# Performance work log

Measured on AMD Instinct MI355X. Metric: run time of the kernel, lower is better.

Reference implementation:

```python
import jax, jax.numpy as jnp
import numpy as np

B, T, D = 4, 4096, 768      # batch, tokens, n_embd
S = 1024                    # memory_slots (divides T -> adaptive pool == window mean)
K = 8                       # memory_topk
RW = 0.1                    # memory_retrieval_weight


def setup_inputs() -> dict:
    key = jax.random.key(0)
    ks = jax.random.split(key, 10)
    w = 1.0 / np.sqrt(D).astype(np.float32)
    return {
        "x": jax.random.normal(ks[0], (B, T, D), jnp.float32),
        "Wq": jax.random.normal(ks[1], (D, D), jnp.float32) * w,
        "bq": jnp.zeros((D,), jnp.float32),
        "Wk": jax.random.normal(ks[2], (D, D), jnp.float32) * w,
        "bk": jnp.zeros((D,), jnp.float32),
        "Wv": jax.random.normal(ks[3], (D, D), jnp.float32) * w,
        "bv": jnp.zeros((D,), jnp.float32),
        "Wp": jax.random.normal(ks[4], (D, D), jnp.float32) * w,
        "bp": jnp.zeros((D,), jnp.float32),
        "persistent_memory": jax.random.normal(ks[5], (S, D), jnp.float32),
    }


def reference(x, Wq, bq, Wk, bk, Wv, bv, Wp, bp, persistent_memory):
    # _build_memory_slots: adaptive_avg_pool1d to S slots; T % S == 0 so it is a window mean
    pooled = x.reshape(B, S, T // S, D).mean(axis=2)                    # [B,S,D]
    pers = jnp.broadcast_to(persistent_memory[None], (B, S, D))         # persistent bank
    slots = jnp.concatenate([pooled, pers], axis=1)                     # [B,2S,D]

    q = x @ Wq + bq                                                     # [B,T,D]
    k = slots @ Wk + bk                                                 # [B,2S,D]
    v = slots @ Wv + bv                                                 # [B,2S,D]

    scores = jnp.einsum('btd,bsd->bts', q, k) / jnp.sqrt(jnp.float32(D))  # [B,T,2S]
    top_s, top_i = jax.lax.top_k(scores, K)                             # [B,T,K]
    w = jax.nn.softmax(top_s, axis=-1)                                  # softmax over top-k only

    # gather top-k values: [B,T,K,D]
    vg = jnp.take_along_axis(v, top_i.reshape(B, T * K)[:, :, None], axis=1)
    vg = vg.reshape(B, T, K, D)
    retrieved = jnp.einsum('btk,btkd->btd', w, vg)                      # weighted combine

    return RW * (retrieved @ Wp + bp)                                   # proj * retrieval_weight
```

## Files before the change

kernel.cpp:

```cpp
#include <hip/hip_runtime.h>
#include <math.h>

#define BB 4
#define TT 4096
#define DD 768
#define SS 1024
#define S2 2048
#define KTOP 8
#define RWEIGHT 0.1f
#define TAU 2e-4f
#define AMB_CAP 256

typedef __attribute__((ext_vector_type(8))) _Float16 f16x8;
typedef __attribute__((ext_vector_type(4))) float f32x4;
typedef _Float16 f16;

__global__ __launch_bounds__(256) void build_pooled_all(
    const float* __restrict__ x, float* __restrict__ slots)
{
    int i = blockIdx.x * 256 + threadIdx.x;
    int s2 = i / DD;
    int d = i - s2 * DD;
    int b = s2 >> 10, s = s2 & 1023;
    const float* xb = x + (size_t)b * TT * DD + (size_t)(4 * s) * DD + d;
    slots[i] = 0.25f * (xb[0] + xb[DD] + xb[2 * DD] + xb[3 * DD]);
}

__global__ __launch_bounds__(256) void transpose_split(
    const float* __restrict__ W0, const float* __restrict__ W1,
    const float* __restrict__ W2, const float* __restrict__ W3,
    f16* __restrict__ WQh, f16* __restrict__ WQm,
    f16* __restrict__ WKh, f16* __restrict__ WKm,
    f16* __restrict__ WVh, f16* __restrict__ WPh,
    float* __restrict__ WkT32)
{
    const int z = blockIdx.z;
    const float* W = (z == 0) ? W0 : (z == 1) ? W1 : (z == 2) ? W2 : W3;
    __shared__ float t[32][33];
    int bx = blockIdx.x * 32, by = blockIdx.y * 32;
    int lx = threadIdx.x & 31, ly = threadIdx.x >> 5;
#pragma unroll
    for (int r = 0; r < 32; r += 8)
        t[ly + r][lx] = W[(size_t)(bx + ly + r) * 768 + by + lx];
    __syncthreads();
#pragma unroll
    for (int r = 0; r < 32; r += 8) {
        float w = t[lx][ly + r];
        size_t idx = (size_t)(by + ly + r) * 768 + bx + lx;
        f16 h = (f16)w;
        if (z == 0) { WQh[idx] = h; WQm[idx] = (f16)(w - (float)h); }
        else if (z == 1) { WKh[idx] = h; WKm[idx] = (f16)(w - (float)h); WkT32[idx] = w; }
        else if (z == 2) { WVh[idx] = h; }
        else { WPh[idx] = h; }
    }
}

__global__ void zeroN(int* p) { p[threadIdx.x] = 0; }

__device__ __forceinline__ void tile_split_prod(
    const float* __restrict__ A, int arow0,
    const f16* __restrict__ Bh, const f16* __restrict__ Bm, int bncol,
    const float* __restrict__ bias,
    f16* __restrict__ Ch, f16* __restrict__ Cm, int crow0,
    f16* LAh, f16* LAm, f16* LBh, f16* LBm)
{
    const int tid = threadIdx.x;
    const int lane = tid & 63;
    const int wc = (tid >> 6) & 1;
    const int wr = (tid >> 7) & 1;
    const int srow = tid >> 1, c0 = tid & 1;
    const int p0 = c0 ^ (srow & 3) ^ ((srow >> 2) & 1);
    const int wo0 = srow * 32 + p0 * 8, wo1 = wo0 ^ 16;
    const int csw = (((lane >> 4) ^ (lane & 3) ^ ((lane >> 2) & 1)) * 8);
    const size_t bn = (size_t)bncol;

    f32x4 acc[4][4];
#pragma unroll
    for (int i = 0; i < 4; ++i)
#pragma unroll
        for (int j = 0; j < 4; ++j) acc[i][j] = (f32x4){0.f, 0.f, 0.f, 0.f};

    const float* pa = A + (size_t)(arow0 + srow) * 768 + c0 * 8;
    const f16* pbh = Bh + (bn + srow) * 768 + c0 * 8;
    const f16* pbm = Bm + (bn + srow) * 768 + c0 * 8;

    for (int k0 = 0; k0 < 768; k0 += 32) {
        float4 a0 = *(const float4*)(pa + k0);
        float4 a1 = *(const float4*)(pa + k0 + 4);
        float4 a2 = *(const float4*)(pa + k0 + 16);
        float4 a3 = *(const float4*)(pa + k0 + 20);
        f16x8 bh0 = *(const f16x8*)(pbh + k0);
        f16x8 bh1 = *(const f16x8*)(pbh + k0 + 16);
        f16x8 bm0 = *(const f16x8*)(pbm + k0);
        f16x8 bm1 = *(const f16x8*)(pbm + k0 + 16);
        __syncthreads();
        {
            float av[16] = {a0.x, a0.y, a0.z, a0.w, a1.x, a1.y, a1.z, a1.w,
                            a2.x, a2.y, a2.z, a2.w, a3.x, a3.y, a3.z, a3.w};
            f16x8 h, m;
#pragma unroll
            for (int j = 0; j < 8; ++j) {
                f16 hh = (f16)av[j]; h[j] = hh; m[j] = (f16)(av[j] - (float)hh);
            }
            *(f16x8*)&LAh[wo0] = h; *(f16x8*)&LAm[wo0] = m;
#pragma unroll
            for (int j = 0; j < 8; ++j) {
                f16 hh = (f16)av[j + 8]; h[j] = hh; m[j] = (f16)(av[j + 8] - (float)hh);
            }
            *(f16x8*)&LAh[wo1] = h; *(f16x8*)&LAm[wo1] = m;
            *(f16x8*)&LBh[wo0] = bh0; *(f16x8*)&LBh[wo1] = bh1;
            *(f16x8*)&LBm[wo0] = bm0; *(f16x8*)&LBm[wo1] = bm1;
        }
        __syncthreads();

        f16x8 fah[4], fam[4], fbh[4], fbm[4];
#pragma unroll
        for (int mi = 0; mi < 4; ++mi) {
            int off = (wr * 64 + mi * 16 + (lane & 15)) * 32 + csw;
            fah[mi] = *(const f16x8*)&LAh[off];
            fam[mi] = *(const f16x8*)&LAm[off];
        }
#pragma unroll
        for (int ni = 0; ni < 4; ++ni) {
            int off = (wc * 64 + ni * 16 + (lane & 15)) * 32 + csw;
            fbh[ni] = *(const f16x8*)&LBh[off];
            fbm[ni] = *(const f16x8*)&LBm[off];
        }
#pragma unroll
        for (int mi = 0; mi < 4; ++mi)
#pragma unroll
            for (int ni = 0; ni < 4; ++ni) {
                acc[mi][ni] = __builtin_amdgcn_mfma_f32_16x16x32_f16(
                    fah[mi], fbh[ni], acc[mi][ni], 0, 0, 0);
                acc[mi][ni] = __builtin_amdgcn_mfma_f32_16x16x32_f16(
                    fah[mi], fbm[ni], acc[mi][ni], 0, 0, 0);
                acc[mi][ni] = __builtin_amdgcn_mfma_f32_16x16x32_f16(
                    fam[mi], fbh[ni], acc[mi][ni], 0, 0, 0);
            }
    }

    const int orow0 = wr * 64 + (lane >> 4) * 4;
    const int ocol0 = wc * 64 + (lane & 15);
#pragma unroll
    for (int mi = 0; mi < 4; ++mi)
#pragma unroll
        for (int ni = 0; ni < 4; ++ni) {
            size_t col = bn + ocol0 + ni * 16;
            float badd = bias[col];
            size_t rbase = (size_t)crow0 + orow0 + mi * 16;
#pragma unroll
            for (int r = 0; r < 4; ++r) {
                float val = acc[mi][ni][r] + badd;
                f16 h = (f16)val;
                size_t idx = (rbase + r) * 768 + col;
                Ch[idx] = h;
                Cm[idx] = (f16)(val - (float)h);
            }
        }
}

__device__ __forceinline__ void tile_1p_prod(
    const float* __restrict__ A, int arow0,
    const f16* __restrict__ Bh, int bncol,
    const float* __restrict__ bias,
    f16* __restrict__ Co, int crow0, f16* LA, f16* LB)
{
    const int tid = threadIdx.x;
    const int lane = tid & 63;
    const int wc = (tid >> 6) & 1;
    const int wr = (tid >> 7) & 1;
    const int srow = tid >> 1, c0 = tid & 1;
    const int p0 = c0 ^ (srow & 3) ^ ((srow >> 2) & 1);
    const int wo0 = srow * 32 + p0 * 8, wo1 = wo0 ^ 16;
    const int csw = (((lane >> 4) ^ (lane & 3) ^ ((lane >> 2) & 1)) * 8);
    const size_t bn = (size_t)bncol;

    f32x4 acc[4][4];
#pragma unroll
    for (int i = 0; i < 4; ++i)
#pragma unroll
        for (int j = 0; j < 4; ++j) acc[i][j] = (f32x4){0.f, 0.f, 0.f, 0.f};

    const float* pa = A + (size_t)(arow0 + srow) * 768 + c0 * 8;
    const f16* pbh = Bh + (bn + srow) * 768 + c0 * 8;

    for (int k0 = 0; k0 < 768; k0 += 32) {
        float4 a0 = *(const float4*)(pa + k0);
        float4 a1 = *(const float4*)(pa + k0 + 4);
        float4 a2 = *(const float4*)(pa + k0 + 16);
        float4 a3 = *(const float4*)(pa + k0 + 20);
        f16x8 bh0 = *(const f16x8*)(pbh + k0);
        f16x8 bh1 = *(const f16x8*)(pbh + k0 + 16);
        __syncthreads();
        {
            f16x8 h;
            h[0] = (f16)a0.x; h[1] = (f16)a0.y; h[2] = (f16)a0.z; h[3] = (f16)a0.w;
            h[4] = (f16)a1.x; h[5] = (f16)a1.y; h[6] = (f16)a1.z; h[7] = (f16)a1.w;
            *(f16x8*)&LA[wo0] = h;
            h[0] = (f16)a2.x; h[1] = (f16)a2.y; h[2] = (f16)a2.z; h[3] = (f16)a2.w;
            h[4] = (f16)a3.x; h[5] = (f16)a3.y; h[6] = (f16)a3.z; h[7] = (f16)a3.w;
            *(f16x8*)&LA[wo1] = h;
            *(f16x8*)&LB[wo0] = bh0;
            *(f16x8*)&LB[wo1] = bh1;
        }
        __syncthreads();
        f16x8 fah[4], fbh[4];
#pragma unroll
        for (int mi = 0; mi < 4; ++mi)
            fah[mi] = *(const f16x8*)&LA[(wr * 64 + mi * 16 + (lane & 15)) * 32 + csw];
#pragma unroll
        for (int ni = 0; ni < 4; ++ni)
            fbh[ni] = *(const f16x8*)&LB[(wc * 64 + ni * 16 + (lane & 15)) * 32 + csw];
#pragma unroll
        for (int mi = 0; mi < 4; ++mi)
#pragma unroll
            for (int ni = 0; ni < 4; ++ni)
                acc[mi][ni] = __builtin_amdgcn_mfma_f32_16x16x32_f16(
                    fah[mi], fbh[ni], acc[mi][ni], 0, 0, 0);
    }

    const int orow0 = wr * 64 + (lane >> 4) * 4;
    const int ocol0 = wc * 64 + (lane & 15);
#pragma unroll
    for (int mi = 0; mi < 4; ++mi)
#pragma unroll
        for (int ni = 0; ni < 4; ++ni) {
            size_t col = bn + ocol0 + ni * 16;
            float badd = bias[col];
            size_t rbase = (size_t)crow0 + orow0 + mi * 16;
#pragma unroll
            for (int r = 0; r < 4; ++r)
                Co[(rbase + r) * 768 + col] = (f16)(acc[mi][ni][r] + badd);
        }
}

__device__ __forceinline__ void tile_proj(
    const f16* __restrict__ A, int arow0,
    const f16* __restrict__ Bh, int bncol,
    const float* __restrict__ bias,
    float* __restrict__ Co, int crow0, f16* LA, f16* LB)
{
    const int tid = threadIdx.x;
    const int lane = tid & 63;
    const int wc = (tid >> 6) & 1;
    const int wr = (tid >> 7) & 1;
    const int srow = tid >> 1, c0 = tid & 1;
    const int p0 = c0 ^ (srow & 3) ^ ((srow >> 2) & 1);
    const int wo0 = srow * 32 + p0 * 8, wo1 = wo0 ^ 16;
    const int csw = (((lane >> 4) ^ (lane & 3) ^ ((lane >> 2) & 1)) * 8);
    const size_t bn = (size_t)bncol;

    f32x4 acc[4][4];
#pragma unroll
    for (int i = 0; i < 4; ++i)
#pragma unroll
        for (int j = 0; j < 4; ++j) acc[i][j] = (f32x4){0.f, 0.f, 0.f, 0.f};

    const f16* pa = A + (size_t)(arow0 + srow) * 768 + c0 * 8;
    const f16* pbh = Bh + (bn + srow) * 768 + c0 * 8;

    for (int k0 = 0; k0 < 768; k0 += 32) {
        f16x8 ah0 = *(const f16x8*)(pa + k0);
        f16x8 ah1 = *(const f16x8*)(pa + k0 + 16);
        f16x8 bh0 = *(const f16x8*)(pbh + k0);
        f16x8 bh1 = *(const f16x8*)(pbh + k0 + 16);
        __syncthreads();
        *(f16x8*)&LA[wo0] = ah0; *(f16x8*)&LA[wo1] = ah1;
        *(f16x8*)&LB[wo0] = bh0; *(f16x8*)&LB[wo1] = bh1;
        __syncthreads();
        f16x8 fah[4], fbh[4];
#pragma unroll
        for (int mi = 0; mi < 4; ++mi)
            fah[mi] = *(const f16x8*)&LA[(wr * 64 + mi * 16 + (lane & 15)) * 32 + csw];
#pragma unroll
        for (int ni = 0; ni < 4; ++ni)
            fbh[ni] = *(const f16x8*)&LB[(wc * 64 + ni * 16 + (lane & 15)) * 32 + csw];
#pragma unroll
        for (int mi = 0; mi < 4; ++mi)
#pragma unroll
            for (int ni = 0; ni < 4; ++ni)
                acc[mi][ni] = __builtin_amdgcn_mfma_f32_16x16x32_f16(
                    fah[mi], fbh[ni], acc[mi][ni], 0, 0, 0);
    }

    const int orow0 = wr * 64 + (lane >> 4) * 4;
    const int ocol0 = wc * 64 + (lane & 15);
#pragma unroll
    for (int mi = 0; mi < 4; ++mi)
#pragma unroll
        for (int ni = 0; ni < 4; ++ni) {
            size_t col = bn + ocol0 + ni * 16;
            float badd = RWEIGHT * bias[col];
            size_t rbase = (size_t)crow0 + orow0 + mi * 16;
#pragma unroll
            for (int r = 0; r < 4; ++r)
                Co[(rbase + r) * 768 + col] = RWEIGHT * acc[mi][ni][r] + badd;
        }
}

__device__ __forceinline__ void tile_scores_planes(
    const f16* __restrict__ qh, const f16* __restrict__ qm, int arow0,
    const f16* __restrict__ kh, const f16* __restrict__ km, int bncol,
    float* __restrict__ C, float alpha,
    f16* LAh, f16* LAm, f16* LBh, f16* LBm)
{
    const int tid = threadIdx.x;
    const int lane = tid & 63;
    const int wc = (tid >> 6) & 1;
    const int wr = (tid >> 7) & 1;
    const int srow = tid >> 1, c0 = tid & 1;
    const int p0 = c0 ^ (srow & 3) ^ ((srow >> 2) & 1);
    const int wo0 = srow * 32 + p0 * 8, wo1 = wo0 ^ 16;
    const int csw = (((lane >> 4) ^ (lane & 3) ^ ((lane >> 2) & 1)) * 8);
    const size_t bn = (size_t)bncol;

    f32x4 acc[4][4];
#pragma unroll
    for (int i = 0; i < 4; ++i)
#pragma unroll
        for (int j = 0; j < 4; ++j) acc[i][j] = (f32x4){0.f, 0.f, 0.f, 0.f};

    const f16* pah = qh + (size_t)(arow0 + srow) * 768 + c0 * 8;
    const f16* pam = qm + (size_t)(arow0 + srow) * 768 + c0 * 8;
    const f16* pbh = kh + (bn + srow) * 768 + c0 * 8;
    const f16* pbm = km + (bn + srow) * 768 + c0 * 8;

    for (int k0 = 0; k0 < 768; k0 += 32) {
        f16x8 ah0 = *(const f16x8*)(pah + k0);
        f16x8 ah1 = *(const f16x8*)(pah + k0 + 16);
        f16x8 am0 = *(const f16x8*)(pam + k0);
        f16x8 am1 = *(const f16x8*)(pam + k0 + 16);
        f16x8 bh0 = *(const f16x8*)(pbh + k0);
        f16x8 bh1 = *(const f16x8*)(pbh + k0 + 16);
        f16x8 bm0 = *(const f16x8*)(pbm + k0);
        f16x8 bm1 = *(const f16x8*)(pbm + k0 + 16);
        __syncthreads();
        *(f16x8*)&LAh[wo0] = ah0; *(f16x8*)&LAh[wo1] = ah1;
        *(f16x8*)&LAm[wo0] = am0; *(f16x8*)&LAm[wo1] = am1;
        *(f16x8*)&LBh[wo0] = bh0; *(f16x8*)&LBh[wo1] = bh1;
        *(f16x8*)&LBm[wo0] = bm0; *(f16x8*)&LBm[wo1] = bm1;
        __syncthreads();

        f16x8 fah[4], fam[4], fbh[4], fbm[4];
#pragma unroll
        for (int mi = 0; mi < 4; ++mi) {
            int off = (wr * 64 + mi * 16 + (lane & 15)) * 32 + csw;
            fah[mi] = *(const f16x8*)&LAh[off];
            fam[mi] = *(const f16x8*)&LAm[off];
        }
#pragma unroll
        for (int ni = 0; ni < 4; ++ni) {
            int off = (wc * 64 + ni * 16 + (lane & 15)) * 32 + csw;
            fbh[ni] = *(const f16x8*)&LBh[off];
            fbm[ni] = *(const f16x8*)&LBm[off];
        }
#pragma unroll
        for (int mi = 0; mi < 4; ++mi)
#pragma unroll
            for (int ni = 0; ni < 4; ++ni) {
                acc[mi][ni] = __builtin_amdgcn_mfma_f32_16x16x32_f16(
                    fah[mi], fbh[ni], acc[mi][ni], 0, 0, 0);
                acc[mi][ni] = __builtin_amdgcn_mfma_f32_16x16x32_f16(
                    fah[mi], fbm[ni], acc[mi][ni], 0, 0, 0);
                acc[mi][ni] = __builtin_amdgcn_mfma_f32_16x16x32_f16(
                    fam[mi], fbh[ni], acc[mi][ni], 0, 0, 0);
            }
    }

    const int orow0 = wr * 64 + (lane >> 4) * 4;
    const int ocol0 = wc * 64 + (lane & 15);
#pragma unroll
    for (int mi = 0; mi < 4; ++mi)
#pragma unroll
        for (int ni = 0; ni < 4; ++ni) {
            size_t col = bn + ocol0 + ni * 16;
            size_t rbase = (size_t)arow0 + orow0 + mi * 16;
#pragma unroll
            for (int r = 0; r < 4; ++r)
                C[(rbase + r) * S2 + col] = alpha * acc[mi][ni][r];
        }
}

__global__ __launch_bounds__(256) void megaSelProd(
    int nSel, const float* __restrict__ scores, const f16* __restrict__ v16r,
    f16* __restrict__ retrW, int gbase,
    int* __restrict__ ambc, int* __restrict__ ambgrow, int* __restrict__ cand,
    float* __restrict__ oldw, f16* __restrict__ vsave,
    int hasQ, int hasKV, int doPm,
    const float* __restrict__ xq, const float* __restrict__ slots_b,
    const float* __restrict__ pm,
    const f16* __restrict__ WQh, const f16* __restrict__ WQm,
    const f16* __restrict__ WKh, const f16* __restrict__ WKm,
    const f16* __restrict__ WVh,
    const float* __restrict__ bq, const float* __restrict__ bk,
    const float* __restrict__ bv,
    f16* __restrict__ qh, f16* __restrict__ qm,
    f16* __restrict__ kh, f16* __restrict__ km,
    f16* __restrict__ v16w, f16* __restrict__ v16w2)
{
    __shared__ f16 LAh[4096], LAm[4096], LBh[4096], LBm[4096];
    int t = blockIdx.x;

    if (hasQ) {
        if (t < 192) {
            tile_split_prod(xq, (t / 6) * 128, WQh, WQm, (t % 6) * 128, bq,
                            qh, qm, (t / 6) * 128, LAh, LAm, LBh, LBm);
            return;
        }
        t -= 192;
    }
    if (hasKV) {
        if (t < 48) {
            tile_split_prod(slots_b, (t / 6) * 128, WKh, WKm, (t % 6) * 128, bk,
                            kh, km, (t / 6) * 128, LAh, LAm, LBh, LBm);
            return;
        }
        t -= 48;
        if (doPm) {
            if (t < 48) {
                tile_split_prod(pm, (t / 6) * 128, WKh, WKm, (t % 6) * 128, bk,
                                kh, km, 1024 + (t / 6) * 128, LAh, LAm, LBh, LBm);
                return;
            }
            t -= 48;
        }
        if (t < 48) {
            tile_1p_prod(slots_b, (t / 6) * 128, WVh, (t % 6) * 128, bv,
                         v16w, (t / 6) * 128, LAh, LBh);
            return;
        }
        t -= 48;
        if (doPm) {
            if (t < 48) {
                tile_1p_prod(pm, (t / 6) * 128, WVh, (t % 6) * 128, bv,
                             v16w, 1024 + (t / 6) * 128, LAh, LBh);
                return;
            }
            t -= 48;
            if (t < 48) {
                tile_1p_prod(pm, (t / 6) * 128, WVh, (t % 6) * 128, bv,
                             v16w2, 1024 + (t / 6) * 128, LAh, LBh);
                return;
            }
            t -= 48;
        }
    }
    if (t >= nSel) return;

    const int lane = threadIdx.x & 63;
    const int wave = threadIdx.x >> 6;
    const int row = t * 4 + wave;
    const float* srow = scores + (size_t)row * S2;
    float vals[32];
#pragma unroll
    for (int i = 0; i < 32; ++i) vals[i] = srow[lane + (i << 6)];

    float topv[16]; int topi[16];
    bool amb = false;
    int nr = 9;
    for (int r = 0; r < 16; ++r) {
        if (r >= nr) break;
        float bvv = -3.4e38f; int bii = 0x7fffffff;
#pragma unroll
        for (int i = 0; i < 32; ++i)
            if (vals[i] > bvv) { bvv = vals[i]; bii = lane + (i << 6); }
#pragma unroll
        for (int off = 32; off > 0; off >>= 1) {
            float ov = __shfl_xor(bvv, off);
            int   oi = __shfl_xor(bii, off);
            if (ov > bvv || (ov == bvv && oi < bii)) { bvv = ov; bii = oi; }
        }
        topv[r] = bvv; topi[r] = bii;
        if ((bii & 63) == lane) vals[bii >> 6] = -3.4e38f;
        if (r == 8) {
            amb = (topv[7] - topv[8]) < TAU;
            if (amb) nr = 16;
        }
    }

    float m = topv[0], w[KTOP], sum = 0.f;
#pragma unroll
    for (int r = 0; r < KTOP; ++r) { w[r] = expf(topv[r] - m); sum += w[r]; }
    float inv = 1.f / sum;
#pragma unroll
    for (int r = 0; r < KTOP; ++r) w[r] *= inv;

    if (amb) {
        int idx = 0;
        if (lane == 0) idx = atomicAdd(ambc, 1);
        idx = __shfl(idx, 0);
        if (idx < AMB_CAP) {
            if (lane == 0) ambgrow[idx] = gbase + row;
            if (lane < 16) cand[idx * 16 + lane] = topi[lane];
            if (lane < KTOP) oldw[idx * KTOP + lane] = w[lane];
            f16* vs = vsave + (size_t)idx * 16 * 768;
            for (int cc = lane; cc < 16 * 96; cc += 64) {
                int cr = cc / 96, ch = cc - cr * 96;
                *(f16x8*)&vs[(size_t)cr * 768 + ch * 8] =
                    *(const f16x8*)&v16r[(size_t)topi[cr] * 768 + ch * 8];
            }
        }
    }

    for (int c = lane; c < 96; c += 64) {
        float o[8] = {0, 0, 0, 0, 0, 0, 0, 0};
#pragma unroll
        for (int r = 0; r < KTOP; ++r) {
            f16x8 vv = *(const f16x8*)&v16r[(size_t)topi[r] * 768 + c * 8];
#pragma unroll
            for (int j = 0; j < 8; ++j) o[j] += w[r] * (float)vv[j];
        }
        f16x8 hx;
#pragma unroll
        for (int j = 0; j < 8; ++j) hx[j] = (f16)o[j];
        *(f16x8*)&retrW[(size_t)row * 768 + c * 8] = hx;
    }
}

__global__ __launch_bounds__(256) void megaScoresProj(
    int nSc, const f16* __restrict__ qh, const f16* __restrict__ qm,
    const f16* __restrict__ kh, const f16* __restrict__ km,
    float* __restrict__ scores, float alpha,
    const f16* __restrict__ retrR, const f16* __restrict__ WPh,
    const float* __restrict__ bp, float* __restrict__ outp)
{
    __shared__ f16 LAh[4096], LAm[4096], LBh[4096], LBm[4096];
    int t = blockIdx.x;
    if (t < nSc) {
        tile_scores_planes(qh, qm, (t >> 4) * 128, kh, km, (t & 15) * 128,
                           scores, alpha, LAh, LAm, LBh, LBm);
        return;
    }
    t -= nSc;
    tile_proj(retrR, (t / 6) * 128, WPh, (t % 6) * 128, bp,
              outp, (t / 6) * 128, LAh, LBh);
}

__global__ __launch_bounds__(256) void fixA(
    const int* __restrict__ amb_count, const int* __restrict__ amb_grow,
    const float* __restrict__ x, const float* __restrict__ Wq,
    const float* __restrict__ bq, double* __restrict__ q64buf)
{
    int n = *amb_count; if (n > AMB_CAP) n = AMB_CAP;
    const int i = blockIdx.y;
    if (i >= n) return;
    const int tid = threadIdx.x;
    const int jl = tid & 63;
    const int ks = tid >> 6;
    const int j = blockIdx.x * 64 + jl;
    const int grow = amb_grow[i];

    __shared__ float xs[768];
    __shared__ double ps[4][64];
    for (int t = tid; t < 768; t += 256) xs[t] = x[(size_t)grow * 768 + t];
    __syncthreads();

    double a0 = 0.0, a1 = 0.0;
    const float* wp = Wq + j;
    const int k0 = ks * 192;
#pragma unroll 8
    for (int k = 0; k < 192; k += 2) {
        a0 = fma((double)xs[k0 + k],     (double)wp[(size_t)(k0 + k) * 768],     a0);
        a1 = fma((double)xs[k0 + k + 1], (double)wp[(size_t)(k0 + k + 1) * 768], a1);
    }
    ps[ks][jl] = a0 + a1;
    __syncthreads();
    if (ks == 0)
        q64buf[(size_t)i * 768 + j] =
            ((ps[0][jl] + ps[1][jl]) + (ps[2][jl] + ps[3][jl])) + (double)bq[j];
}

__global__ __launch_bounds__(256) void fixB(
    const int* __restrict__ amb_count,
    const float* __restrict__ WkT, const float* __restrict__ bk,
    const double* __restrict__ q64buf,
    double* __restrict__ ubuf, double* __restrict__ bkqbuf)
{
    int n = *amb_count; if (n > AMB_CAP) n = AMB_CAP;
    const int i = blockIdx.y;
    if (i >= n) return;
    const int tid = threadIdx.x;
    const int tl = tid & 63;
    const int js = tid >> 6;
    const int t = blockIdx.x * 64 + tl;

    __shared__ double qs[768];
    __shared__ double ps[4][64];
    const double* qrow = q64buf + (size_t)i * 768;
    for (int k = tid; k < 768; k += 256) qs[k] = qrow[k];
    __syncthreads();

    double a0 = 0.0, a1 = 0.0;
    const float* wp = WkT + t;
    const int j0 = js * 192;
#pragma unroll 8
    for (int k = 0; k < 192; k += 2) {
        a0 = fma((double)wp[(size_t)(j0 + k) * 768],     qs[j0 + k],     a0);
        a1 = fma((double)wp[(size_t)(j0 + k + 1) * 768], qs[j0 + k + 1], a1);
    }
    ps[js][tl] = a0 + a1;
    __syncthreads();
    if (js == 0)
        ubuf[(size_t)i * 768 + t] = (ps[0][tl] + ps[1][tl]) + (ps[2][tl] + ps[3][tl]);

    if (blockIdx.x == 0 && tid < 64) {
        double p = 0.0;
#pragma unroll
        for (int c = 0; c < 12; ++c) {
            int jj = tid + (c << 6);
            p = fma((double)bk[jj], qs[jj], p);
        }
#pragma unroll
        for (int off = 32; off; off >>= 1) p += __shfl_xor(p, off);
        if (tid == 0) bkqbuf[i] = p;
    }
}

__global__ __launch_bounds__(256) void fixC(
    const int* __restrict__ amb_count, const int* __restrict__ amb_grow,
    const float* __restrict__ x, const float* __restrict__ pm,
    const int* __restrict__ cand, const float* __restrict__ oldw,
    const double* __restrict__ ubuf, const double* __restrict__ bkqbuf,
    const f16* __restrict__ vsave, float* __restrict__ dret)
{
    int n = *amb_count; if (n > AMB_CAP) n = AMB_CAP;
    const int i = blockIdx.x;
    if (i >= n) return;
    const int tid = threadIdx.x;
    const int lane = tid & 63;
    const int wave = tid >> 6;
    const int grow = amb_grow[i];
    const float* xb = x + (size_t)(grow >> 12) * TT * 768;

    __shared__ double us[768];
    __shared__ double cs_s[16];
    __shared__ float coef[16];

    const double* urow = ubuf + (size_t)i * 768;
    for (int t = tid; t < 768; t += 256) us[t] = urow[t];
    __syncthreads();

    const double ISQ = 1.0 / sqrt((double)DD);
    const double bkq = bkqbuf[i];
#pragma unroll
    for (int c = wave; c < 16; c += 4) {
        int s = cand[i * 16 + c];
        double p = 0.0;
        if (s < SS) {
            const float* xr = xb + (size_t)(4 * s) * 768;
#pragma unroll
            for (int t = 0; t < 12; ++t) {
                int j2 = lane + (t << 6);
                double sv = 0.25 * ((double)xr[j2] + (double)xr[j2 + 768] +
                                    (double)xr[j2 + 1536] + (double)xr[j2 + 2304]);
                p = fma(sv, us[j2], p);
            }
        } else {
            const float* pr = pm + (size_t)(s - SS) * 768;
#pragma unroll
            for (int t = 0; t < 12; ++t) {
                int j2 = lane + (t << 6);
                p = fma((double)pr[j2], us[j2], p);
            }
        }
#pragma unroll
        for (int off = 32; off; off >>= 1) p += __shfl_xor(p, off);
        if (lane == 0) cs_s[c] = (p + bkq) * ISQ;
    }
    __syncthreads();

    if (tid == 0) {
        double cs[16]; int ci[16];
        for (int c = 0; c < 16; ++c) { cs[c] = cs_s[c]; ci[c] = cand[i * 16 + c]; }
        unsigned used = 0;
        double sv[KTOP]; int sp[KTOP];
        for (int r = 0; r < KTOP; ++r) {
            int bi = -1;
            for (int c = 0; c < 16; ++c) {
                if (used & (1u << c)) continue;
                if (bi < 0 || cs[c] > cs[bi] ||
                    (cs[c] == cs[bi] && ci[c] < ci[bi])) bi = c;
            }
            used |= (1u << bi); sv[r] = cs[bi]; sp[r] = bi;
        }
        double mx = sv[0], es[KTOP], ssum = 0.0;
        for (int r = 0; r < KTOP; ++r) { es[r] = exp(sv[r] - mx); ssum += es[r]; }
        for (int c = 0; c < 16; ++c) coef[c] = (c < KTOP) ? -oldw[i * KTOP + c] : 0.f;
        for (int r = 0; r < KTOP; ++r) coef[sp[r]] += (float)(es[r] / ssum);
    }
    __syncthreads();

    const f16* vs = vsave + (size_t)i * 16 * 768;
    for (int j = tid; j < 768; j += 256) {
        float d = 0.f;
#pragma unroll
        for (int c = 0; c < 16; ++c) d += coef[c] * (float)vs[(size_t)c * 768 + j];
        dret[(size_t)i * 768 + j] = d;
    }
}

__global__ __launch_bounds__(256) void fixD(
    const int* __restrict__ amb_count, const int* __restrict__ amb_grow,
    const float* __restrict__ dret, const float* __restrict__ Wp,
    float* __restrict__ out)
{
    int n = *amb_count; if (n > AMB_CAP) n = AMB_CAP;
    const int i = blockIdx.y;
    if (i >= n) return;
    const int tid = threadIdx.x;
    const int jl = tid & 63;
    const int ks = tid >> 6;
    const int j = blockIdx.x * 64 + jl;
    const int grow = amb_grow[i];

    __shared__ float ds[768];
    __shared__ float ps[4][64];
    for (int t = tid; t < 768; t += 256) ds[t] = dret[(size_t)i * 768 + t];
    __syncthreads();

    float a0 = 0.f, a1 = 0.f;
    const float* wp = Wp + j;
    const int k0 = ks * 192;
#pragma unroll 8
    for (int k = 0; k < 192; k += 2) {
        a0 = fmaf(ds[k0 + k],     wp[(size_t)(k0 + k) * 768],     a0);
        a1 = fmaf(ds[k0 + k + 1], wp[(size_t)(k0 + k + 1) * 768], a1);
    }
    ps[ks][jl] = a0 + a1;
    __syncthreads();
    if (ks == 0)
        out[(size_t)grow * 768 + j] +=
            RWEIGHT * ((ps[0][jl] + ps[1][jl]) + (ps[2][jl] + ps[3][jl]));
}

extern "C" void kernel_launch(void* const* d_in, const int* in_sizes, int n_in,
                              void* d_out, int out_size, void* d_ws, size_t ws_size,
                              hipStream_t stream)
{
    const float* x  = (const float*)d_in[0];
    const float* Wq = (const float*)d_in[1];
    const float* bq = (const float*)d_in[2];
    const float* Wk = (const float*)d_in[3];
    const float* bk = (const float*)d_in[4];
    const float* Wv = (const float*)d_in[5];
    const float* bv = (const float*)d_in[6];
    const float* Wp = (const float*)d_in[7];
    const float* bp = (const float*)d_in[8];
    const float* pm = (const float*)d_in[9];
    float* out = (float*)d_out;
    float* ws  = (float*)d_ws;

    const float inv_sqrt_d = (float)(1.0 / sqrt((double)DD));
    const size_t TD  = (size_t)TT * DD;
    const size_t SD  = (size_t)SS * DD;
    const size_t WSZ = (size_t)DD * DD;

    float* p = ws;
    f16* WQh = (f16*)p; p += WSZ / 2;
    f16* WQm = (f16*)p; p += WSZ / 2;
    f16* WKh = (f16*)p; p += WSZ / 2;
    f16* WKm = (f16*)p; p += WSZ / 2;
    f16* WVh = (f16*)p; p += WSZ / 2;
    f16* WPh = (f16*)p; p += WSZ / 2;
    float* WkT32 = p; p += WSZ;
    float* slots_all = p; p += (size_t)BB * SD;
    f16* qh = (f16*)p; p += TD / 2;
    f16* qm = (f16*)p; p += TD / 2;
    f16* kh = (f16*)p; p += SD;
    f16* km = (f16*)p; p += SD;
    f16* v16a = (f16*)p; p += SD;
    f16* v16b = (f16*)p; p += SD;
    f16* retrA = (f16*)p; p += TD / 2;
    f16* retrB = (f16*)p; p += TD / 2;
    double* q64buf = (double*)p; p += (size_t)AMB_CAP * DD * 2;
    double* ubuf   = (double*)p; p += (size_t)AMB_CAP * DD * 2;
    double* bkqbuf = (double*)p; p += AMB_CAP * 2;
    int* cand = (int*)p; p += (size_t)AMB_CAP * 16;
    float* oldw = p; p += (size_t)AMB_CAP * KTOP;
    f16* vsave = (f16*)p; p += (size_t)AMB_CAP * 16 * DD / 2;
    float* dret = p; p += (size_t)AMB_CAP * DD;
    int* ambc = (int*)p; p += 64;
    int* ambgrow = (int*)p; p += AMB_CAP;
    float* scores = p;

    transpose_split<<<dim3(24, 24, 4), 256, 0, stream>>>(
        Wq, Wk, Wv, Wp, WQh, WQm, WKh, WKm, WVh, WPh, WkT32);
    zeroN<<<1, 64, 0, stream>>>(ambc);
    build_pooled_all<<<(BB * SS * DD) / 256, 256, 0, stream>>>(x, slots_all);

    megaSelProd<<<432, 256, 0, stream>>>(
        0, nullptr, nullptr, nullptr, 0, ambc, ambgrow, cand, oldw, vsave,
        1, 1, 1, x, slots_all, pm,
        WQh, WQm, WKh, WKm, WVh, bq, bk, bv, qh, qm, kh, km, v16a, v16b);
    megaScoresProj<<<512, 256, 0, stream>>>(
        512, qh, qm, kh, km, scores, inv_sqrt_d, nullptr, WPh, bp, nullptr);

    for (int b = 1; b < BB; ++b) {
        f16* v16w = (b & 1) ? v16b : v16a;
        f16* v16r = ((b - 1) & 1) ? v16b : v16a;
        f16* retrW = ((b - 1) & 1) ? retrB : retrA;

        megaSelProd<<<1312, 256, 0, stream>>>(
            1024, scores, v16r, retrW, (b - 1) * TT,
            ambc, ambgrow, cand, oldw, vsave,
            1, 1, 0, x + (size_t)b * TD, slots_all + (size_t)b * SD, nullptr,
            WQh, WQm, WKh, WKm, WVh, bq, bk, bv, qh, qm, kh, km, v16w, nullptr);
        megaScoresProj<<<704, 256, 0, stream>>>(
            512, qh, qm, kh, km, scores, inv_sqrt_d,
            retrW, WPh, bp, out + (size_t)(b - 1) * TD);
    }

    f16* v16r3 = v16b;
    f16* retrW3 = retrB;
    megaSelProd<<<1024, 256, 0, stream>>>(
        1024, scores, v16r3, retrW3, 3 * TT,
        ambc, ambgrow, cand, oldw, vsave,
        0, 0, 0, nullptr, nullptr, nullptr,
        WQh, WQm, WKh, WKm, WVh, bq, bk, bv, qh, qm, kh, km, nullptr, nullptr);
    megaScoresProj<<<192, 256, 0, stream>>>(
        0, nullptr, nullptr, nullptr, nullptr, nullptr, 0.f,
        retrW3, WPh, bp, out + (size_t)3 * TD);

    fixA<<<dim3(12, AMB_CAP), 256, 0, stream>>>(ambc, ambgrow, x, Wq, bq, q64buf);
    fixB<<<dim3(12, AMB_CAP), 256, 0, stream>>>(ambc, WkT32, bk, q64buf, ubuf, bkqbuf);
    fixC<<<AMB_CAP, 256, 0, stream>>>(ambc, ambgrow, x, pm, cand, oldw,
                                      ubuf, bkqbuf, vsave, dret);
    fixD<<<dim3(12, AMB_CAP), 256, 0, stream>>>(ambc, ambgrow, dret, Wp, out);
}
```

Before: 643.1 us.

## Drop q low plane from score GEMM, widen ambiguity margin and fixup capacity

The query is now stored as a single fp16 plane, with x converted to fp16 inside the Q projection tile, instead of a hi/lo split pair. This cuts the Q projection and score GEMMs from three MFMA passes to two and removes the qm buffer traffic. The less accurate scores are compensated by a wider top-k ambiguity threshold and a larger cap on rows sent to the fp64 fixup kernels. fixB now reads untransposed Wk with a row stride, so the fp32 transposed copy is no longer needed, and dret is stored as fp16. The cost is more rows handled in the serial fixup kernels, plus fixup grids sized 5x larger. Correctness depends on the fixup path catching every top-k boundary that the lower precision flips.

```diff
diff --git a/kernel.cpp b/kernel.cpp
--- a/kernel.cpp
+++ b/kernel.cpp
@@ -8,8 +8,8 @@
 #define S2 2048
 #define KTOP 8
 #define RWEIGHT 0.1f
-#define TAU 2e-4f
-#define AMB_CAP 256
+#define TAU 2e-3f
+#define AMB_CAP 1280
 
 typedef __attribute__((ext_vector_type(8))) _Float16 f16x8;
 typedef __attribute__((ext_vector_type(4))) float f32x4;
@@ -31,8 +31,7 @@
     const float* __restrict__ W2, const float* __restrict__ W3,
     f16* __restrict__ WQh, f16* __restrict__ WQm,
     f16* __restrict__ WKh, f16* __restrict__ WKm,
-    f16* __restrict__ WVh, f16* __restrict__ WPh,
-    float* __restrict__ WkT32)
+    f16* __restrict__ WVh, f16* __restrict__ WPh)
 {
     const int z = blockIdx.z;
     const float* W = (z == 0) ? W0 : (z == 1) ? W1 : (z == 2) ? W2 : W3;
@@ -49,13 +48,98 @@
         size_t idx = (size_t)(by + ly + r) * 768 + bx + lx;
         f16 h = (f16)w;
         if (z == 0) { WQh[idx] = h; WQm[idx] = (f16)(w - (float)h); }
-        else if (z == 1) { WKh[idx] = h; WKm[idx] = (f16)(w - (float)h); WkT32[idx] = w; }
+        else if (z == 1) { WKh[idx] = h; WKm[idx] = (f16)(w - (float)h); }
         else if (z == 2) { WVh[idx] = h; }
         else { WPh[idx] = h; }
     }
 }
 
 __global__ void zeroN(int* p) { p[threadIdx.x] = 0; }
+
+__device__ __forceinline__ void tile_prod2p_q(
+    const float* __restrict__ A, int arow0,
+    const f16* __restrict__ Bh, const f16* __restrict__ Bm, int bncol,
+    const float* __restrict__ bias,
+    f16* __restrict__ Co, int crow0, f16* LAh, f16* LBh, f16* LBm)
+{
+    const int tid = threadIdx.x;
+    const int lane = tid & 63;
+    const int wc = (tid >> 6) & 1;
+    const int wr = (tid >> 7) & 1;
+    const int srow = tid >> 1, c0 = tid & 1;
+    const int p0 = c0 ^ (srow & 3) ^ ((srow >> 2) & 1);
+    const int wo0 = srow * 32 + p0 * 8, wo1 = wo0 ^ 16;
+    const int csw = (((lane >> 4) ^ (lane & 3) ^ ((lane >> 2) & 1)) * 8);
+    const size_t bn = (size_t)bncol;
+
+    f32x4 acc[4][4];
+#pragma unroll
+    for (int i = 0; i < 4; ++i)
+#pragma unroll
+        for (int j = 0; j < 4; ++j) acc[i][j] = (f32x4){0.f, 0.f, 0.f, 0.f};
+
+    const float* pa = A + (size_t)(arow0 + srow) * 768 + c0 * 8;
+    const f16* pbh = Bh + (bn + srow) * 768 + c0 * 8;
+    const f16* pbm = Bm + (bn + srow) * 768 + c0 * 8;
+
+    for (int k0 = 0; k0 < 768; k0 += 32) {
+        float4 a0 = *(const float4*)(pa + k0);
+        float4 a1 = *(const float4*)(pa + k0 + 4);
+        float4 a2 = *(const float4*)(pa + k0 + 16);
+        float4 a3 = *(const float4*)(pa + k0 + 20);
+        f16x8 bh0 = *(const f16x8*)(pbh + k0);
+        f16x8 bh1 = *(const f16x8*)(pbh + k0 + 16);
+        f16x8 bm0 = *(const f16x8*)(pbm + k0);
+        f16x8 bm1 = *(const f16x8*)(pbm + k0 + 16);
+        __syncthreads();
+        {
+            f16x8 h;
+            h[0] = (f16)a0.x; h[1] = (f16)a0.y; h[2] = (f16)a0.z; h[3] = (f16)a0.w;
+            h[4] = (f16)a1.x; h[5] = (f16)a1.y; h[6] = (f16)a1.z; h[7] = (f16)a1.w;
+            *(f16x8*)&LAh[wo0] = h;
+            h[0] = (f16)a2.x; h[1] = (f16)a2.y; h[2] = (f16)a2.z; h[3] = (f16)a2.w;
+            h[4] = (f16)a3.x; h[5] = (f16)a3.y; h[6] = (f16)a3.z; h[7] = (f16)a3.w;
+            *(f16x8*)&LAh[wo1] = h;
+            *(f16x8*)&LBh[wo0] = bh0; *(f16x8*)&LBh[wo1] = bh1;
+            *(f16x8*)&LBm[wo0] = bm0; *(f16x8*)&LBm[wo1] = bm1;
+        }
+        __syncthreads();
+
+        f16x8 fah[4], fbh[4], fbm[4];
+#pragma unroll
+        for (int mi = 0; mi < 4; ++mi)
+            fah[mi] = *(const f16x8*)&LAh[(wr * 64 + mi * 16 + (lane & 15)) * 32 + csw];
+#pragma unroll
+        for (int ni = 0; ni < 4; ++ni) {
+            int off = (wc * 64 + ni * 16 + (lane & 15)) * 32 + csw;
+            fbh[ni] = *(const f16x8*)&LBh[off];
+            fbm[ni] = *(const f16x8*)&LBm[off];
+        }
+#pragma unroll
+        for (int mi = 0; mi < 4; ++mi)
+#pragma unroll
+            for (int ni = 0; ni < 4; ++ni) {
+                acc[mi][ni] = __builtin_amdgcn_mfma_f32_16x16x32_f16(
+                    fah[mi], fbh[ni], acc[mi][ni], 0, 0, 0);
+                acc[mi][ni] = __builtin_amdgcn_mfma_f32_16x16x32_f16(
+                    fah[mi], fbm[ni], acc[mi][ni], 0, 0, 0);
+            }
+    }
+
+    const int orow0 = wr * 64 + (lane >> 4) * 4;
+    const int ocol0 = wc * 64 + (lane & 15);
+#pragma unroll
+    for (int mi = 0; mi < 4; ++mi)
+#pragma unroll
+        for (int ni = 0; ni < 4; ++ni) {
+            size_t col = bn + ocol0 + ni * 16;
+            float badd = bias[col];
+            size_t rbase = (size_t)crow0 + orow0 + mi * 16;
+#pragma unroll
+            for (int r = 0; r < 4; ++r)
+                Co[(rbase + r) * 768 + col] = (f16)(acc[mi][ni][r] + badd);
+        }
+}
 
 __device__ __forceinline__ void tile_split_prod(
     const float* __restrict__ A, int arow0,
@@ -298,11 +382,11 @@
         }
 }
 
-__device__ __forceinline__ void tile_scores_planes(
-    const f16* __restrict__ qh, const f16* __restrict__ qm, int arow0,
+__device__ __forceinline__ void tile_scores_2p(
+    const f16* __restrict__ qh, int arow0,
     const f16* __restrict__ kh, const f16* __restrict__ km, int bncol,
     float* __restrict__ C, float alpha,
-    f16* LAh, f16* LAm, f16* LBh, f16* LBm)
+    f16* LAh, f16* LBh, f16* LBm)
 {
     const int tid = threadIdx.x;
     const int lane = tid & 63;
@@ -321,33 +405,26 @@
         for (int j = 0; j < 4; ++j) acc[i][j] = (f32x4){0.f, 0.f, 0.f, 0.f};
 
     const f16* pah = qh + (size_t)(arow0 + srow) * 768 + c0 * 8;
-    const f16* pam = qm + (size_t)(arow0 + srow) * 768 + c0 * 8;
     const f16* pbh = kh + (bn + srow) * 768 + c0 * 8;
     const f16* pbm = km + (bn + srow) * 768 + c0 * 8;
 
     for (int k0 = 0; k0 < 768; k0 += 32) {
         f16x8 ah0 = *(const f16x8*)(pah + k0);
         f16x8 ah1 = *(const f16x8*)(pah + k0 + 16);
-        f16x8 am0 = *(const f16x8*)(pam + k0);
-        f16x8 am1 = *(const f16x8*)(pam + k0 + 16);
         f16x8 bh0 = *(const f16x8*)(pbh + k0);
         f16x8 bh1 = *(const f16x8*)(pbh + k0 + 16);
         f16x8 bm0 = *(const f16x8*)(pbm + k0);
         f16x8 bm1 = *(const f16x8*)(pbm + k0 + 16);
         __syncthreads();
         *(f16x8*)&LAh[wo0] = ah0; *(f16x8*)&LAh[wo1] = ah1;
-        *(f16x8*)&LAm[wo0] = am0; *(f16x8*)&LAm[wo1] = am1;
         *(f16x8*)&LBh[wo0] = bh0; *(f16x8*)&LBh[wo1] = bh1;
         *(f16x8*)&LBm[wo0] = bm0; *(f16x8*)&LBm[wo1] = bm1;
         __syncthreads();
 
-        f16x8 fah[4], fam[4], fbh[4], fbm[4];
-#pragma unroll
-        for (int mi = 0; mi < 4; ++mi) {
-            int off = (wr * 64 + mi * 16 + (lane & 15)) * 32 + csw;
-            fah[mi] = *(const f16x8*)&LAh[off];
-            fam[mi] = *(const f16x8*)&LAm[off];
-        }
+        f16x8 fah[4], fbh[4], fbm[4];
+#pragma unroll
+        for (int mi = 0; mi < 4; ++mi)
+            fah[mi] = *(const f16x8*)&LAh[(wr * 64 + mi * 16 + (lane & 15)) * 32 + csw];
 #pragma unroll
         for (int ni = 0; ni < 4; ++ni) {
             int off = (wc * 64 + ni * 16 + (lane & 15)) * 32 + csw;
@@ -362,8 +439,6 @@
                     fah[mi], fbh[ni], acc[mi][ni], 0, 0, 0);
                 acc[mi][ni] = __builtin_amdgcn_mfma_f32_16x16x32_f16(
                     fah[mi], fbm[ni], acc[mi][ni], 0, 0, 0);
-                acc[mi][ni] = __builtin_amdgcn_mfma_f32_16x16x32_f16(
-                    fam[mi], fbh[ni], acc[mi][ni], 0, 0, 0);
             }
     }
 
@@ -394,8 +469,7 @@
     const f16* __restrict__ WVh,
     const float* __restrict__ bq, const float* __restrict__ bk,
     const float* __restrict__ bv,
-    f16* __restrict__ qh, f16* __restrict__ qm,
-    f16* __restrict__ kh, f16* __restrict__ km,
+    f16* __restrict__ qh, f16* __restrict__ kh, f16* __restrict__ km,
     f16* __restrict__ v16w, f16* __restrict__ v16w2)
 {
     __shared__ f16 LAh[4096], LAm[4096], LBh[4096], LBm[4096];
@@ -403,8 +477,8 @@
 
     if (hasQ) {
         if (t < 192) {
-            tile_split_prod(xq, (t / 6) * 128, WQh, WQm, (t % 6) * 128, bq,
-                            qh, qm, (t / 6) * 128, LAh, LAm, LBh, LBm);
+            tile_prod2p_q(xq, (t / 6) * 128, WQh, WQm, (t % 6) * 128, bq,
+                          qh, (t / 6) * 128, LAh, LBh, LBm);
             return;
         }
         t -= 192;
@@ -518,17 +592,17 @@
 }
 
 __global__ __launch_bounds__(256) void megaScoresProj(
-    int nSc, const f16* __restrict__ qh, const f16* __restrict__ qm,
+    int nSc, const f16* __restrict__ qh,
     const f16* __restrict__ kh, const f16* __restrict__ km,
     float* __restrict__ scores, float alpha,
     const f16* __restrict__ retrR, const f16* __restrict__ WPh,
     const float* __restrict__ bp, float* __restrict__ outp)
 {
-    __shared__ f16 LAh[4096], LAm[4096], LBh[4096], LBm[4096];
+    __shared__ f16 LAh[4096], LBh[4096], LBm[4096];
     int t = blockIdx.x;
     if (t < nSc) {
-        tile_scores_planes(qh, qm, (t >> 4) * 128, kh, km, (t & 15) * 128,
-                           scores, alpha, LAh, LAm, LBh, LBm);
+        tile_scores_2p(qh, (t >> 4) * 128, kh, km, (t & 15) * 128,
+                       scores, alpha, LAh, LBh, LBm);
         return;
     }
     t -= nSc;
@@ -572,7 +646,7 @@
 
 __global__ __launch_bounds__(256) void fixB(
     const int* __restrict__ amb_count,
-    const float* __restrict__ WkT, const float* __restrict__ bk,
+    const float* __restrict__ Wk, const float* __restrict__ bk,
     const double* __restrict__ q64buf,
     double* __restrict__ ubuf, double* __restrict__ bkqbuf)
 {
@@ -591,12 +665,12 @@
     __syncthreads();
 
     double a0 = 0.0, a1 = 0.0;
-    const float* wp = WkT + t;
+    const float* wp = Wk + (size_t)t * 768;
     const int j0 = js * 192;
 #pragma unroll 8
     for (int k = 0; k < 192; k += 2) {
-        a0 = fma((double)wp[(size_t)(j0 + k) * 768],     qs[j0 + k],     a0);
-        a1 = fma((double)wp[(size_t)(j0 + k + 1) * 768], qs[j0 + k + 1], a1);
+        a0 = fma((double)wp[j0 + k],     qs[j0 + k],     a0);
+        a1 = fma((double)wp[j0 + k + 1], qs[j0 + k + 1], a1);
     }
     ps[js][tl] = a0 + a1;
     __syncthreads();
@@ -621,7 +695,7 @@
     const float* __restrict__ x, const float* __restrict__ pm,
     const int* __restrict__ cand, const float* __restrict__ oldw,
     const double* __restrict__ ubuf, const double* __restrict__ bkqbuf,
-    const f16* __restrict__ vsave, float* __restrict__ dret)
+    const f16* __restrict__ vsave, f16* __restrict__ dret)
 {
     int n = *amb_count; if (n > AMB_CAP) n = AMB_CAP;
     const int i = blockIdx.x;
@@ -695,13 +769,13 @@
         float d = 0.f;
 #pragma unroll
         for (int c = 0; c < 16; ++c) d += coef[c] * (float)vs[(size_t)c * 768 + j];
-        dret[(size_t)i * 768 + j] = d;
+        dret[(size_t)i * 768 + j] = (f16)d;
     }
 }
 
 __global__ __launch_bounds__(256) void fixD(
     const int* __restrict__ amb_count, const int* __restrict__ amb_grow,
-    const float* __restrict__ dret, const float* __restrict__ Wp,
+    const f16* __restrict__ dret, const float* __restrict__ Wp,
     float* __restrict__ out)
 {
     int n = *amb_count; if (n > AMB_CAP) n = AMB_CAP;
@@ -715,7 +789,7 @@
 
     __shared__ float ds[768];
     __shared__ float ps[4][64];
-    for (int t = tid; t < 768; t += 256) ds[t] = dret[(size_t)i * 768 + t];
+    for (int t = tid; t < 768; t += 256) ds[t] = (float)dret[(size_t)i * 768 + t];
     __syncthreads();
 
     float a0 = 0.f, a1 = 0.f;
@@ -762,10 +836,8 @@
     f16* WKm = (f16*)p; p += WSZ / 2;
     f16* WVh = (f16*)p; p += WSZ / 2;
     f16* WPh = (f16*)p; p += WSZ / 2;
-    float* WkT32 = p; p += WSZ;
     float* slots_all = p; p += (size_t)BB * SD;
     f16* qh = (f16*)p; p += TD / 2;
-    f16* qm = (f16*)p; p += TD / 2;
     f16* kh = (f16*)p; p += SD;
     f16* km = (f16*)p; p += SD;
     f16* v16a = (f16*)p; p += SD;
@@ -778,22 +850,22 @@
     int* cand = (int*)p; p += (size_t)AMB_CAP * 16;
     float* oldw = p; p += (size_t)AMB_CAP * KTOP;
     f16* vsave = (f16*)p; p += (size_t)AMB_CAP * 16 * DD / 2;
-    float* dret = p; p += (size_t)AMB_CAP * DD;
+    f16* dret = (f16*)p; p += (size_t)AMB_CAP * DD / 2;
     int* ambc = (int*)p; p += 64;
     int* ambgrow = (int*)p; p += AMB_CAP;
     float* scores = p;
 
     transpose_split<<<dim3(24, 24, 4), 256, 0, stream>>>(
-        Wq, Wk, Wv, Wp, WQh, WQm, WKh, WKm, WVh, WPh, WkT32);
+        Wq, Wk, Wv, Wp, WQh, WQm, WKh, WKm, WVh, WPh);
     zeroN<<<1, 64, 0, stream>>>(ambc);
     build_pooled_all<<<(BB * SS * DD) / 256, 256, 0, stream>>>(x, slots_all);
 
     megaSelProd<<<432, 256, 0, stream>>>(
         0, nullptr, nullptr, nullptr, 0, ambc, ambgrow, cand, oldw, vsave,
         1, 1, 1, x, slots_all, pm,
-        WQh, WQm, WKh, WKm, WVh, bq, bk, bv, qh, qm, kh, km, v16a, v16b);
+        WQh, WQm, WKh, WKm, WVh, bq, bk, bv, qh, kh, km, v16a, v16b);
     megaScoresProj<<<512, 256, 0, stream>>>(
-        512, qh, qm, kh, km, scores, inv_sqrt_d, nullptr, WPh, bp, nullptr);
+        512, qh, kh, km, scores, inv_sqrt_d, nullptr, WPh, bp, nullptr);
 
     for (int b = 1; b < BB; ++b) {
         f16* v16w = (b & 1) ? v16b : v16a;
@@ -804,9 +876,9 @@
             1024, scores, v16r, retrW, (b - 1) * TT,
             ambc, ambgrow, cand, oldw, vsave,
             1, 1, 0, x + (size_t)b * TD, slots_all + (size_t)b * SD, nullptr,
-            WQh, WQm, WKh, WKm, WVh, bq, bk, bv, qh, qm, kh, km, v16w, nullptr);
+            WQh, WQm, WKh, WKm, WVh, bq, bk, bv, qh, kh, km, v16w, nullptr);
         megaScoresProj<<<704, 256, 0, stream>>>(
-            512, qh, qm, kh, km, scores, inv_sqrt_d,
+            512, qh, kh, km, scores, inv_sqrt_d,
             retrW, WPh, bp, out + (size_t)(b - 1) * TD);
     }
 
@@ -816,13 +888,13 @@
         1024, scores, v16r3, retrW3, 3 * TT,
         ambc, ambgrow, cand, oldw, vsave,
         0, 0, 0, nullptr, nullptr, nullptr,
-        WQh, WQm, WKh, WKm, WVh, bq, bk, bv, qh, qm, kh, km, nullptr, nullptr);
+        WQh, WQm, WKh, WKm, WVh, bq, bk, bv, qh, kh, km, nullptr, nullptr);
     megaScoresProj<<<192, 256, 0, stream>>>(
-        0, nullptr, nullptr, nullptr, nullptr, nullptr, 0.f,
+        0, nullptr, nullptr, nullptr, nullptr, 0.f,
         retrW3, WPh, bp, out + (size_t)3 * TD);
 
     fixA<<<dim3(12, AMB_CAP), 256, 0, stream>>>(ambc, ambgrow, x, Wq, bq, q64buf);
-    fixB<<<dim3(12, AMB_CAP), 256, 0, stream>>>(ambc, WkT32, bk, q64buf, ubuf, bkqbuf);
+    fixB<<<dim3(12, AMB_CAP), 256, 0, stream>>>(ambc, Wk, bk, q64buf, ubuf, bkqbuf);
     fixC<<<AMB_CAP, 256, 0, stream>>>(ambc, ambgrow, x, pm, cand, oldw,
                                       ubuf, bkqbuf, vsave, dret);
     fixD<<<dim3(12, AMB_CAP), 256, 0, stream>>>(ambc, ambgrow, dret, Wp, out);
```

After: 893.4 us. 1.39x slower.
